# Kernel tuning notes

Hardware: AMD Instinct MI355X
Metric: run time of the kernel (lower is better)

The kernel has to match this reference:

```python
import jax, jax.numpy as jnp
import numpy as np


def setup_inputs() -> dict:
    key = jax.random.key(0)
    k1, k2, k3, k4, k5, k6 = jax.random.split(key, 6)
    B, N = 256, 512
    return {
        "node_features": jax.random.normal(k1, (B, N, 2), dtype=jnp.float32),
        "adj_matrices": jax.random.uniform(k2, (B, N, N), dtype=jnp.float32),
        "W1": jax.random.normal(k3, (2, 4), dtype=jnp.float32) * 0.5,
        "b1": jax.random.normal(k4, (4,), dtype=jnp.float32) * 0.1,
        "W2": jax.random.normal(k5, (4, 1), dtype=jnp.float32) * 0.5,
        "b2": jax.random.normal(k6, (1,), dtype=jnp.float32) * 0.1,
    }


def reference(node_features, adj_matrices, W1, b1, W2, b2):
    # GraphConv (1 layer): aggregate neighbors via dense adjacency, linear, ReLU
    agg = jnp.einsum('bnm,bmf->bnf', adj_matrices, node_features)   # [B,N,2]
    h = jax.nn.relu(agg @ W1 + b1)                                   # [B,N,4]
    # dense readout + sum over nodes
    prop = h @ W2 + b2                                               # [B,N,1]
    return jnp.sum(prop, axis=1)                                     # [B,1]
```

## Files before the change

### kernel.cpp

```cpp
#include <hip/hip_runtime.h>

#define BATCH 256
#define NNODE 512

__global__ void init_out_kernel(const float* __restrict__ b2, float* __restrict__ out) {
    int i = blockIdx.x * blockDim.x + threadIdx.x;
    if (i < BATCH) out[i] = (float)NNODE * b2[0];
}

__global__ __launch_bounds__(256) void gcn_main_kernel(
    const float* __restrict__ x,
    const float* __restrict__ adj,
    const float* __restrict__ W1,
    const float* __restrict__ b1,
    const float* __restrict__ W2,
    float* __restrict__ out)
{
    __shared__ __align__(16) float sx0[NNODE];
    __shared__ __align__(16) float sx1[NNODE];
    __shared__ float swsum[4];

    const int b     = blockIdx.x >> 3;
    const int chunk = blockIdx.x & 7;
    const int t     = threadIdx.x;

    {
        const float4 v = ((const float4*)(x + (size_t)b * NNODE * 2))[t];
        const int m = 2 * t;
        sx0[m]     = v.x; sx1[m]     = v.y;
        sx0[m + 1] = v.z; sx1[m + 1] = v.w;
    }

    float w1[8], bb1[4], w2[4];
#pragma unroll
    for (int j = 0; j < 8; ++j) w1[j] = W1[j];
#pragma unroll
    for (int j = 0; j < 4; ++j) { bb1[j] = b1[j]; w2[j] = W2[j]; }

    __syncthreads();

    const int wave = t >> 6;
    const int lane = t & 63;
    const int sub  = lane >> 4;
    const int l    = lane & 15;

    float acc = 0.0f;
    const int row_base = chunk * 64 + wave * 16;

#pragma unroll 1
    for (int it = 0; it < 4; ++it) {
        const int n = row_base + it * 4 + sub;
        const float4* __restrict__ arow =
            (const float4*)(adj + ((size_t)b * NNODE + n) * NNODE);

        float a0 = 0.0f, a1 = 0.0f;
#pragma unroll
        for (int k = 0; k < 8; ++k) {
            const int c = l + k * 16;
            const float4 av  = arow[c];
            const float4 xv0 = ((const float4*)sx0)[c];
            const float4 xv1 = ((const float4*)sx1)[c];
            a0 += av.x * xv0.x + av.y * xv0.y + av.z * xv0.z + av.w * xv0.w;
            a1 += av.x * xv1.x + av.y * xv1.y + av.z * xv1.z + av.w * xv1.w;
        }

#pragma unroll
        for (int m = 1; m < 16; m <<= 1) {
            a0 += __shfl_xor(a0, m, 64);
            a1 += __shfl_xor(a1, m, 64);
        }

        float p = 0.0f;
#pragma unroll
        for (int j = 0; j < 4; ++j) {
            float h = a0 * w1[j] + a1 * w1[4 + j] + bb1[j];
            h = fmaxf(h, 0.0f);
            p += h * w2[j];
        }
        if (l == 0) acc += p;
    }

#pragma unroll
    for (int m = 1; m < 64; m <<= 1) acc += __shfl_xor(acc, m, 64);
    if (lane == 0) swsum[wave] = acc;
    __syncthreads();
    if (t == 0) {
        atomicAdd(out + b, swsum[0] + swsum[1] + swsum[2] + swsum[3]);
    }
}

extern "C" void kernel_launch(void* const* d_in, const int* in_sizes, int n_in,
                              void* d_out, int out_size, void* d_ws, size_t ws_size,
                              hipStream_t stream) {
    const float* x   = (const float*)d_in[0];
    const float* adj = (const float*)d_in[1];
    const float* W1  = (const float*)d_in[2];
    const float* b1  = (const float*)d_in[3];
    const float* W2  = (const float*)d_in[4];
    const float* b2  = (const float*)d_in[5];
    float* out = (float*)d_out;

    hipLaunchKernelGGL(init_out_kernel, dim3(1), dim3(256), 0, stream, b2, out);
    hipLaunchKernelGGL(gcn_main_kernel, dim3(BATCH * 8), dim3(256), 0, stream,
                       x, adj, W1, b1, W2, out);
}
```

Measured before the change: 365.3 us.

## Fully unroll row loop to issue all adjacency loads at once with nontemporal hints

Replaces the serial four-iteration row loop with a single unrolled pass in which each 16-lane group handles four consecutive rows, so 32 float4 loads per thread can be in flight together instead of 8. Adjacency loads use nontemporal hints because the streamed matrix is never reused, and launch bounds now request 4 blocks per CU. The shuffle reductions are batched across the four rows. The goal is more memory-level parallelism in a bandwidth-bound stream, at the cost of higher register pressure.

Result: faster. 347.1 us (-5.0%).

```diff
diff --git a/kernel.cpp b/kernel.cpp
--- a/kernel.cpp
+++ b/kernel.cpp
@@ -2,13 +2,15 @@
 
 #define BATCH 256
 #define NNODE 512
+
+typedef float floatx4 __attribute__((ext_vector_type(4)));
 
 __global__ void init_out_kernel(const float* __restrict__ b2, float* __restrict__ out) {
     int i = blockIdx.x * blockDim.x + threadIdx.x;
     if (i < BATCH) out[i] = (float)NNODE * b2[0];
 }
 
-__global__ __launch_bounds__(256) void gcn_main_kernel(
+__global__ __launch_bounds__(256, 4) void gcn_main_kernel(
     const float* __restrict__ x,
     const float* __restrict__ adj,
     const float* __restrict__ W1,
@@ -44,40 +46,48 @@
     const int sub  = lane >> 4;
     const int l    = lane & 15;
 
-    float acc = 0.0f;
-    const int row_base = chunk * 64 + wave * 16;
+    const int row0 = chunk * 64 + wave * 16 + sub * 4;
+    const floatx4* __restrict__ arow =
+        (const floatx4*)(adj + ((size_t)b * NNODE + row0) * NNODE);
 
-#pragma unroll 1
-    for (int it = 0; it < 4; ++it) {
-        const int n = row_base + it * 4 + sub;
-        const float4* __restrict__ arow =
-            (const float4*)(adj + ((size_t)b * NNODE + n) * NNODE);
-
-        float a0 = 0.0f, a1 = 0.0f;
-#pragma unroll
-        for (int k = 0; k < 8; ++k) {
-            const int c = l + k * 16;
-            const float4 av  = arow[c];
-            const float4 xv0 = ((const float4*)sx0)[c];
-            const float4 xv1 = ((const float4*)sx1)[c];
-            a0 += av.x * xv0.x + av.y * xv0.y + av.z * xv0.z + av.w * xv0.w;
-            a1 += av.x * xv1.x + av.y * xv1.y + av.z * xv1.z + av.w * xv1.w;
-        }
+    float s0[4] = {0.f, 0.f, 0.f, 0.f};
+    float s1[4] = {0.f, 0.f, 0.f, 0.f};
 
 #pragma unroll
-        for (int m = 1; m < 16; m <<= 1) {
-            a0 += __shfl_xor(a0, m, 64);
-            a1 += __shfl_xor(a1, m, 64);
+    for (int k = 0; k < 8; ++k) {
+        const int c = l + k * 16;
+        const floatx4 xv0 = ((const floatx4*)sx0)[c];
+        const floatx4 xv1 = ((const floatx4*)sx1)[c];
+#pragma unroll
+        for (int r = 0; r < 4; ++r) {
+            const floatx4 av = __builtin_nontemporal_load(&arow[(size_t)r * (NNODE / 4) + c]);
+            s0[r] += av.x * xv0.x + av.y * xv0.y + av.z * xv0.z + av.w * xv0.w;
+            s1[r] += av.x * xv1.x + av.y * xv1.y + av.z * xv1.z + av.w * xv1.w;
         }
+    }
 
-        float p = 0.0f;
 #pragma unroll
-        for (int j = 0; j < 4; ++j) {
-            float h = a0 * w1[j] + a1 * w1[4 + j] + bb1[j];
-            h = fmaxf(h, 0.0f);
-            p += h * w2[j];
+    for (int m = 1; m < 16; m <<= 1) {
+#pragma unroll
+        for (int r = 0; r < 4; ++r) {
+            s0[r] += __shfl_xor(s0[r], m, 64);
+            s1[r] += __shfl_xor(s1[r], m, 64);
         }
-        if (l == 0) acc += p;
+    }
+
+    float acc = 0.0f;
+    if (l == 0) {
+#pragma unroll
+        for (int r = 0; r < 4; ++r) {
+            float p = 0.0f;
+#pragma unroll
+            for (int j = 0; j < 4; ++j) {
+                float h = fmaf(s0[r], w1[j], fmaf(s1[r], w1[4 + j], bb1[j]));
+                h = fmaxf(h, 0.0f);
+                p += h * w2[j];
+            }
+            acc += p;
+        }
     }
 
 #pragma unroll
```
